# Optimization experiments

Hardware: AMD Instinct MI355X
Metric: run time of the kernel (lower is better)

## Reference

```python
import jax, jax.numpy as jnp
import numpy as np

DT = 10.0 / 200  # 0.05
DX = 20.0 / 128  # 0.15625

# 5x5 fixed finite-difference stencils (torch Conv2d = cross-correlation, so use as-is)
_LAPL = np.array([[0, 0, -1/12, 0, 0],
                  [0, 0,  4/3,  0, 0],
                  [-1/12, 4/3, -5, 4/3, -1/12],
                  [0, 0,  4/3,  0, 0],
                  [0, 0, -1/12, 0, 0]], dtype=np.float32)
_PAR_X = np.array([[0, 0,  1/12, 0, 0],
                   [0, 0, -8/12, 0, 0],
                   [0, 0,  0,    0, 0],
                   [0, 0,  8/12, 0, 0],
                   [0, 0, -1/12, 0, 0]], dtype=np.float32)


def _conv2d_valid(x, kern):
    # x: [N, 1, H, W], kern: [5, 5] -> [N, 1, H-4, W-4]
    return jax.lax.conv_general_dilated(x, jnp.asarray(kern)[None, None], (1, 1), 'VALID')


def _time_deriv(x):
    # x: [T, B, 1, h, w]; central diff interior, one-sided at endpoints (all /DT)
    interior = (x[2:] - x[:-2]) / (2.0 * DT)
    t0 = (-1.5 * x[0] + 2.0 * x[1] - 0.5 * x[2]) / DT
    tn = (0.5 * x[-3] - 2.0 * x[-2] + 1.5 * x[-1]) / DT
    return jnp.concatenate([t0[None], interior, tn[None]], axis=0)


def setup_inputs() -> dict:
    key = jax.random.key(0)
    output = jax.random.normal(key, (20, 8, 3, 256, 256), dtype=jnp.float32)
    return {"output": output}


def reference(output):
    T, B, C, H, W = output.shape
    u = output[:, :, 1:2]  # [T,B,1,H,W]
    v = output[:, :, 2:3]

    lap_u = _conv2d_valid(u.reshape(T * B, 1, H, W), _LAPL).reshape(T, B, 1, H - 4, W - 4) / (DX ** 2)
    lap_v = _conv2d_valid(v.reshape(T * B, 1, H, W), _LAPL).reshape(T, B, 1, H - 4, W - 4) / (DX ** 2)

    uc = u[:, :, :, 2:-2, 2:-2]  # [T,B,1,H-4,W-4]
    vc = v[:, :, :, 2:-2, 2:-2]
    u_t = _time_deriv(uc)
    v_t = _time_deriv(vc)

    Du, Dv = 0.16, 0.08
    f, k = 0.06, 0.062
    f_u = Du * lap_u - uc * vc ** 2 + f * (1.0 - uc) - u_t
    f_v = Dv * lap_v + uc * vc ** 2 - (f + k) * vc - v_t
    return (f_u, f_v)
```

## Files before the change

### kernel.cpp

```cpp
#include <hip/hip_runtime.h>


#define T_OUT (8 * 252 * 252)

typedef float vf4 __attribute__((ext_vector_type(4)));

static __device__ __forceinline__ vf4 lds4u(const float* p) {
    vf4 v;
    __builtin_memcpy(&v, p, 16);
    return v;
}

struct GSRow {
    vf4 u_cm2, u_cm1, u_cc, u_lm1, u_l0;
    vf4 v_cm2, v_cm1, v_cc, v_lm1, v_l0;
};

#define GS_INT(c) { \
    float ut = (ucn.c - s.u_cm1.c) * hdt; \
    float vt = (vcn.c - s.v_cm1.c) * hdt; \
    float uvv = s.u_cc.c * s.v_cc.c * s.v_cc.c; \
    fu.c = Du * s.u_lm1.c - uvv + fR * (1.0f - s.u_cc.c) - ut; \
    fv.c = Dv * s.v_lm1.c + uvv - (fR + kR) * s.v_cc.c - vt; }

#define GS_T0(c) { \
    float ut = (-1.5f * s.u_cm1.c + 2.0f * s.u_cc.c - 0.5f * ucn.c) * inv_dt; \
    float vt = (-1.5f * s.v_cm1.c + 2.0f * s.v_cc.c - 0.5f * vcn.c) * inv_dt; \
    float uvv = s.u_cm1.c * s.v_cm1.c * s.v_cm1.c; \
    fu.c = Du * s.u_l0.c - uvv + fR * (1.0f - s.u_cm1.c) - ut; \
    fv.c = Dv * s.v_l0.c + uvv - (fR + kR) * s.v_cm1.c - vt; }

#define GS_TN(c) { \
    float ut = (0.5f * s.u_cm2.c - 2.0f * s.u_cm1.c + 1.5f * s.u_cc.c) * inv_dt; \
    float vt = (0.5f * s.v_cm2.c - 2.0f * s.v_cm1.c + 1.5f * s.v_cc.c) * inv_dt; \
    float uvv = s.u_cc.c * s.v_cc.c * s.v_cc.c; \
    fu.c = Du * s.u_lm1.c - uvv + fR * (1.0f - s.u_cc.c) - ut; \
    fv.c = Dv * s.v_lm1.c + uvv - (fR + kR) * s.v_cc.c - vt; }

static __device__ __forceinline__ void gs_step(
    const float (*L)[256], int R, int x0, int t, GSRow& s, bool act,
    float* __restrict__ outu, float* __restrict__ outv)
{
    const float C1 = 4.0f / 3.0f, C2 = 1.0f / 12.0f;
    const float inv_dx2 = 1.0f / (0.15625f * 0.15625f);
    const float inv_dt  = 20.0f;
    const float hdt     = 10.0f;
    const float Du = 0.16f, Dv = 0.08f, fR = 0.06f, kR = 0.062f;

    vf4 uL  = *(const vf4*)&L[R + 2][x0];
    vf4 uR  = *(const vf4*)&L[R + 2][x0 + 4];
    vf4 um1 = lds4u(&L[R + 1][x0 + 2]);
    vf4 up1 = lds4u(&L[R + 3][x0 + 2]);
    vf4 um2 = lds4u(&L[R    ][x0 + 2]);
    vf4 up2 = lds4u(&L[R + 4][x0 + 2]);

    vf4 vL  = *(const vf4*)&L[R + 14][x0];
    vf4 vR  = *(const vf4*)&L[R + 14][x0 + 4];
    vf4 vm1 = lds4u(&L[R + 13][x0 + 2]);
    vf4 vp1 = lds4u(&L[R + 15][x0 + 2]);
    vf4 vm2 = lds4u(&L[R + 12][x0 + 2]);
    vf4 vp2 = lds4u(&L[R + 16][x0 + 2]);

    vf4 lu, lv;
    lu.x = (C1*(uL.y + uL.w + um1.x + up1.x) - C2*(uL.x + uR.x + um2.x + up2.x) - 5.0f*uL.z) * inv_dx2;
    lu.y = (C1*(uL.z + uR.x + um1.y + up1.y) - C2*(uL.y + uR.y + um2.y + up2.y) - 5.0f*uL.w) * inv_dx2;
    lu.z = (C1*(uL.w + uR.y + um1.z + up1.z) - C2*(uL.z + uR.z + um2.z + up2.z) - 5.0f*uR.x) * inv_dx2;
    lu.w = (C1*(uR.x + uR.z + um1.w + up1.w) - C2*(uL.w + uR.w + um2.w + up2.w) - 5.0f*uR.y) * inv_dx2;
    lv.x = (C1*(vL.y + vL.w + vm1.x + vp1.x) - C2*(vL.x + vR.x + vm2.x + vp2.x) - 5.0f*vL.z) * inv_dx2;
    lv.y = (C1*(vL.z + vR.x + vm1.y + vp1.y) - C2*(vL.y + vR.y + vm2.y + vp2.y) - 5.0f*vL.w) * inv_dx2;
    lv.z = (C1*(vL.w + vR.y + vm1.z + vp1.z) - C2*(vL.z + vR.z + vm2.z + vp2.z) - 5.0f*vR.x) * inv_dx2;
    lv.w = (C1*(vR.x + vR.z + vm1.w + vp1.w) - C2*(vL.w + vR.w + vm2.w + vp2.w) - 5.0f*vR.y) * inv_dx2;

    vf4 ucn = {uL.z, uL.w, uR.x, uR.y};
    vf4 vcn = {vL.z, vL.w, vR.x, vR.y};

    if (t == 0) { s.u_l0 = lu; s.v_l0 = lv; }

    if (t == 2 && act) {
        vf4 fu, fv;
        GS_T0(x); GS_T0(y); GS_T0(z); GS_T0(w);
        __builtin_nontemporal_store(fu, (vf4*)(outu));
        __builtin_nontemporal_store(fv, (vf4*)(outv));
    }

    if (t >= 2 && act) {
        vf4 fu, fv;
        GS_INT(x); GS_INT(y); GS_INT(z); GS_INT(w);
        __builtin_nontemporal_store(fu, (vf4*)(outu + (size_t)(t - 1) * T_OUT));
        __builtin_nontemporal_store(fv, (vf4*)(outv + (size_t)(t - 1) * T_OUT));
    }

    s.u_cm2 = s.u_cm1; s.u_cm1 = s.u_cc; s.u_cc = ucn; s.u_lm1 = lu;
    s.v_cm2 = s.v_cm1; s.v_cm1 = s.v_cc; s.v_cc = vcn; s.v_lm1 = lv;
}

static __device__ __forceinline__ void gs_tail(
    GSRow& s, bool act, float* __restrict__ outu, float* __restrict__ outv)
{
    const float inv_dt = 20.0f;
    const float Du = 0.16f, Dv = 0.08f, fR = 0.06f, kR = 0.062f;
    if (!act) return;
    vf4 fu, fv;
    GS_TN(x); GS_TN(y); GS_TN(z); GS_TN(w);
    __builtin_nontemporal_store(fu, (vf4*)(outu + (size_t)19 * T_OUT));
    __builtin_nontemporal_store(fv, (vf4*)(outv + (size_t)19 * T_OUT));
}

__global__ __launch_bounds__(256, 1) void gs_loss_kernel(
    const float* __restrict__ in, float* __restrict__ out)
{
    __shared__ float lds[2][24][256];

    const int tid = threadIdx.x;
    const int w   = tid >> 6;
    const int ln  = tid & 63;

    const int b     = blockIdx.x & 7;
    const int ytile = blockIdx.x >> 3;
    const int y0    = ytile * 8;

    const int planeStride = 256 * 256;
    const int bStride     = 3 * planeStride;
    const int tStride     = 24 * planeStride;

    const int col = ln * 4;
    const float* base0 = in + (size_t)b * bStride + planeStride;

    const int gr0 = y0 + w;
    const int gr1 = (y0 + w + 4 < 256) ? (y0 + w + 4) : 255;
    const int gr2 = (y0 + w + 8 < 256) ? (y0 + w + 8) : 255;
    const size_t r0 = (size_t)gr0 * 256 + col;
    const size_t r1 = (size_t)gr1 * 256 + col;
    const size_t r2 = (size_t)gr2 * 256 + col;

    const int x0 = ln * 4;
    const bool active = (ln < 63);
    const bool act2   = active && (y0 + w + 4 < 252);

    const int total = 20 * T_OUT;
    float* outu1 = out + ((size_t)b * 252 + (y0 + w)) * 252 + x0;
    float* outv1 = outu1 + total;
    const int y2 = act2 ? (y0 + w + 4) : (y0 + w);
    float* outu2 = out + ((size_t)b * 252 + y2) * 252 + x0;
    float* outv2 = outu2 + total;

    GSRow s1{}, s2{};

    vf4 sA0, sA1, sA2, sA3, sA4, sA5;
    vf4 sB0, sB1, sB2, sB3, sB4, sB5;

#define ISSUE_A(t) { const float* bt = base0 + (size_t)(t) * tStride; \
    sA0 = *(const vf4*)(bt + r0); \
    sA1 = *(const vf4*)(bt + r1); \
    sA2 = *(const vf4*)(bt + r2); \
    sA3 = *(const vf4*)(bt + planeStride + r0); \
    sA4 = *(const vf4*)(bt + planeStride + r1); \
    sA5 = *(const vf4*)(bt + planeStride + r2); }
#define ISSUE_B(t) { const float* bt = base0 + (size_t)(t) * tStride; \
    sB0 = *(const vf4*)(bt + r0); \
    sB1 = *(const vf4*)(bt + r1); \
    sB2 = *(const vf4*)(bt + r2); \
    sB3 = *(const vf4*)(bt + planeStride + r0); \
    sB4 = *(const vf4*)(bt + planeStride + r1); \
    sB5 = *(const vf4*)(bt + planeStride + r2); }

    ISSUE_A(0);
    ISSUE_B(1);

#pragma unroll
    for (int t = 0; t < 20; ++t) {
        float (*L)[256] = lds[t & 1];

        if ((t & 1) == 0) {
            *(vf4*)&L[w     ][col] = sA0;
            *(vf4*)&L[w + 4 ][col] = sA1;
            *(vf4*)&L[w + 8 ][col] = sA2;
            *(vf4*)&L[w + 12][col] = sA3;
            *(vf4*)&L[w + 16][col] = sA4;
            *(vf4*)&L[w + 20][col] = sA5;
        } else {
            *(vf4*)&L[w     ][col] = sB0;
            *(vf4*)&L[w + 4 ][col] = sB1;
            *(vf4*)&L[w + 8 ][col] = sB2;
            *(vf4*)&L[w + 12][col] = sB3;
            *(vf4*)&L[w + 16][col] = sB4;
            *(vf4*)&L[w + 20][col] = sB5;
        }

        __syncthreads();

        if (t + 2 < 20) {
            if ((t & 1) == 0) { ISSUE_A(t + 2); } else { ISSUE_B(t + 2); }
        }

        gs_step(L, w,     x0, t, s1, active, outu1, outv1);
        gs_step(L, w + 4, x0, t, s2, act2,   outu2, outv2);
    }

    gs_tail(s1, active, outu1, outv1);
    gs_tail(s2, act2,   outu2, outv2);
}

extern "C" void kernel_launch(void* const* d_in, const int* in_sizes, int n_in,
                              void* d_out, int out_size, void* d_ws, size_t ws_size,
                              hipStream_t stream) {
    const float* in = (const float*)d_in[0];
    float* out = (float*)d_out;

    gs_loss_kernel<<<8 * 32, 256, 0, stream>>>(in, out);
}
```

Baseline: 189.5 us.

## Split tiles into column halves, one output row per thread, doubling grid size

```diff
diff --git a/kernel.cpp b/kernel.cpp
--- a/kernel.cpp
+++ b/kernel.cpp
@@ -38,7 +38,7 @@
     fv.c = Dv * s.v_lm1.c + uvv - (fR + kR) * s.v_cc.c - vt; }
 
 static __device__ __forceinline__ void gs_step(
-    const float (*L)[256], int R, int x0, int t, GSRow& s, bool act,
+    const float (*L)[132], int R, int a0, int t, GSRow& s,
     float* __restrict__ outu, float* __restrict__ outv)
 {
     const float C1 = 4.0f / 3.0f, C2 = 1.0f / 12.0f;
@@ -47,19 +47,19 @@
     const float hdt     = 10.0f;
     const float Du = 0.16f, Dv = 0.08f, fR = 0.06f, kR = 0.062f;
 
-    vf4 uL  = *(const vf4*)&L[R + 2][x0];
-    vf4 uR  = *(const vf4*)&L[R + 2][x0 + 4];
-    vf4 um1 = lds4u(&L[R + 1][x0 + 2]);
-    vf4 up1 = lds4u(&L[R + 3][x0 + 2]);
-    vf4 um2 = lds4u(&L[R    ][x0 + 2]);
-    vf4 up2 = lds4u(&L[R + 4][x0 + 2]);
-
-    vf4 vL  = *(const vf4*)&L[R + 14][x0];
-    vf4 vR  = *(const vf4*)&L[R + 14][x0 + 4];
-    vf4 vm1 = lds4u(&L[R + 13][x0 + 2]);
-    vf4 vp1 = lds4u(&L[R + 15][x0 + 2]);
-    vf4 vm2 = lds4u(&L[R + 12][x0 + 2]);
-    vf4 vp2 = lds4u(&L[R + 16][x0 + 2]);
+    vf4 uL  = *(const vf4*)&L[R + 2][a0];
+    vf4 uR  = *(const vf4*)&L[R + 2][a0 + 4];
+    vf4 um1 = lds4u(&L[R + 1][a0 + 2]);
+    vf4 up1 = lds4u(&L[R + 3][a0 + 2]);
+    vf4 um2 = lds4u(&L[R    ][a0 + 2]);
+    vf4 up2 = lds4u(&L[R + 4][a0 + 2]);
+
+    vf4 vL  = *(const vf4*)&L[R + 14][a0];
+    vf4 vR  = *(const vf4*)&L[R + 14][a0 + 4];
+    vf4 vm1 = lds4u(&L[R + 13][a0 + 2]);
+    vf4 vp1 = lds4u(&L[R + 15][a0 + 2]);
+    vf4 vm2 = lds4u(&L[R + 12][a0 + 2]);
+    vf4 vp2 = lds4u(&L[R + 16][a0 + 2]);
 
     vf4 lu, lv;
     lu.x = (C1*(uL.y + uL.w + um1.x + up1.x) - C2*(uL.x + uR.x + um2.x + up2.x) - 5.0f*uL.z) * inv_dx2;
@@ -76,14 +76,14 @@
 
     if (t == 0) { s.u_l0 = lu; s.v_l0 = lv; }
 
-    if (t == 2 && act) {
+    if (t == 2) {
         vf4 fu, fv;
         GS_T0(x); GS_T0(y); GS_T0(z); GS_T0(w);
         __builtin_nontemporal_store(fu, (vf4*)(outu));
         __builtin_nontemporal_store(fv, (vf4*)(outv));
     }
 
-    if (t >= 2 && act) {
+    if (t >= 2) {
         vf4 fu, fv;
         GS_INT(x); GS_INT(y); GS_INT(z); GS_INT(w);
         __builtin_nontemporal_store(fu, (vf4*)(outu + (size_t)(t - 1) * T_OUT));
@@ -94,97 +94,82 @@
     s.v_cm2 = s.v_cm1; s.v_cm1 = s.v_cc; s.v_cc = vcn; s.v_lm1 = lv;
 }
 
-static __device__ __forceinline__ void gs_tail(
-    GSRow& s, bool act, float* __restrict__ outu, float* __restrict__ outv)
-{
-    const float inv_dt = 20.0f;
-    const float Du = 0.16f, Dv = 0.08f, fR = 0.06f, kR = 0.062f;
-    if (!act) return;
-    vf4 fu, fv;
-    GS_TN(x); GS_TN(y); GS_TN(z); GS_TN(w);
-    __builtin_nontemporal_store(fu, (vf4*)(outu + (size_t)19 * T_OUT));
-    __builtin_nontemporal_store(fv, (vf4*)(outv + (size_t)19 * T_OUT));
-}
-
-__global__ __launch_bounds__(256, 1) void gs_loss_kernel(
+__global__ __launch_bounds__(256) void gs_loss_kernel(
     const float* __restrict__ in, float* __restrict__ out)
 {
-    __shared__ float lds[2][24][256];
+    __shared__ float lds[2][24][132];
 
     const int tid = threadIdx.x;
-    const int w   = tid >> 6;
-    const int ln  = tid & 63;
 
     const int b     = blockIdx.x & 7;
-    const int ytile = blockIdx.x >> 3;
+    const int xh    = (blockIdx.x >> 3) & 1;
+    const int ytile = blockIdx.x >> 4;
     const int y0    = ytile * 8;
 
     const int planeStride = 256 * 256;
     const int bStride     = 3 * planeStride;
     const int tStride     = 24 * planeStride;
 
-    const int col = ln * 4;
     const float* base0 = in + (size_t)b * bStride + planeStride;
 
-    const int gr0 = y0 + w;
-    const int gr1 = (y0 + w + 4 < 256) ? (y0 + w + 4) : 255;
-    const int gr2 = (y0 + w + 8 < 256) ? (y0 + w + 8) : 255;
-    const size_t r0 = (size_t)gr0 * 256 + col;
-    const size_t r1 = (size_t)gr1 * 256 + col;
-    const size_t r2 = (size_t)gr2 * 256 + col;
-
-    const int x0 = ln * 4;
-    const bool active = (ln < 63);
-    const bool act2   = active && (y0 + w + 4 < 252);
+    const bool s3 = (tid < 24);
+    int goffs[4], loffs[4];
+#pragma unroll
+    for (int i = 0; i < 4; ++i) {
+        int idx = tid + 256 * i;
+        if (idx >= 792) idx = 791;
+        int r  = idx / 33;
+        int g  = idx - r * 33;
+        int pr = (r < 12) ? r : r - 12;
+        int pl = (r < 12) ? 0 : 1;
+        int gy = y0 + pr; if (gy > 255) gy = 255;
+        goffs[i] = pl * planeStride + gy * 256 + xh * 124 + g * 4;
+        loffs[i] = r * 132 + g * 4;
+    }
+
+    const int R  = tid >> 5;
+    const int cg = tid & 31;
+    const int c0 = xh * 128 + cg * 4;
+    const int a0 = cg * 4 + 4 * xh;
+    const bool act = (c0 <= 248) && (y0 + R < 252);
 
     const int total = 20 * T_OUT;
-    float* outu1 = out + ((size_t)b * 252 + (y0 + w)) * 252 + x0;
-    float* outv1 = outu1 + total;
-    const int y2 = act2 ? (y0 + w + 4) : (y0 + w);
-    float* outu2 = out + ((size_t)b * 252 + y2) * 252 + x0;
-    float* outv2 = outu2 + total;
-
-    GSRow s1{}, s2{};
-
-    vf4 sA0, sA1, sA2, sA3, sA4, sA5;
-    vf4 sB0, sB1, sB2, sB3, sB4, sB5;
+    float* outu = out + ((size_t)b * 252 + (y0 + R)) * 252 + c0;
+    float* outv = outu + total;
+
+    GSRow s{};
+
+    vf4 sA0, sA1, sA2, sA3;
+    vf4 sB0, sB1, sB2, sB3;
 
 #define ISSUE_A(t) { const float* bt = base0 + (size_t)(t) * tStride; \
-    sA0 = *(const vf4*)(bt + r0); \
-    sA1 = *(const vf4*)(bt + r1); \
-    sA2 = *(const vf4*)(bt + r2); \
-    sA3 = *(const vf4*)(bt + planeStride + r0); \
-    sA4 = *(const vf4*)(bt + planeStride + r1); \
-    sA5 = *(const vf4*)(bt + planeStride + r2); }
+    sA0 = *(const vf4*)(bt + goffs[0]); \
+    sA1 = *(const vf4*)(bt + goffs[1]); \
+    sA2 = *(const vf4*)(bt + goffs[2]); \
+    if (s3) sA3 = *(const vf4*)(bt + goffs[3]); }
 #define ISSUE_B(t) { const float* bt = base0 + (size_t)(t) * tStride; \
-    sB0 = *(const vf4*)(bt + r0); \
-    sB1 = *(const vf4*)(bt + r1); \
-    sB2 = *(const vf4*)(bt + r2); \
-    sB3 = *(const vf4*)(bt + planeStride + r0); \
-    sB4 = *(const vf4*)(bt + planeStride + r1); \
-    sB5 = *(const vf4*)(bt + planeStride + r2); }
+    sB0 = *(const vf4*)(bt + goffs[0]); \
+    sB1 = *(const vf4*)(bt + goffs[1]); \
+    sB2 = *(const vf4*)(bt + goffs[2]); \
+    if (s3) sB3 = *(const vf4*)(bt + goffs[3]); }
 
     ISSUE_A(0);
     ISSUE_B(1);
 
 #pragma unroll
     for (int t = 0; t < 20; ++t) {
-        float (*L)[256] = lds[t & 1];
+        float* Lf = &lds[t & 1][0][0];
 
         if ((t & 1) == 0) {
-            *(vf4*)&L[w     ][col] = sA0;
-            *(vf4*)&L[w + 4 ][col] = sA1;
-            *(vf4*)&L[w + 8 ][col] = sA2;
-            *(vf4*)&L[w + 12][col] = sA3;
-            *(vf4*)&L[w + 16][col] = sA4;
-            *(vf4*)&L[w + 20][col] = sA5;
+            *(vf4*)(Lf + loffs[0]) = sA0;
+            *(vf4*)(Lf + loffs[1]) = sA1;
+            *(vf4*)(Lf + loffs[2]) = sA2;
+            if (s3) *(vf4*)(Lf + loffs[3]) = sA3;
         } else {
-            *(vf4*)&L[w     ][col] = sB0;
-            *(vf4*)&L[w + 4 ][col] = sB1;
-            *(vf4*)&L[w + 8 ][col] = sB2;
-            *(vf4*)&L[w + 12][col] = sB3;
-            *(vf4*)&L[w + 16][col] = sB4;
-            *(vf4*)&L[w + 20][col] = sB5;
+            *(vf4*)(Lf + loffs[0]) = sB0;
+            *(vf4*)(Lf + loffs[1]) = sB1;
+            *(vf4*)(Lf + loffs[2]) = sB2;
+            if (s3) *(vf4*)(Lf + loffs[3]) = sB3;
         }
 
         __syncthreads();
@@ -193,12 +178,19 @@
             if ((t & 1) == 0) { ISSUE_A(t + 2); } else { ISSUE_B(t + 2); }
         }
 
-        gs_step(L, w,     x0, t, s1, active, outu1, outv1);
-        gs_step(L, w + 4, x0, t, s2, act2,   outu2, outv2);
-    }
-
-    gs_tail(s1, active, outu1, outv1);
-    gs_tail(s2, act2,   outu2, outv2);
+        if (act) {
+            gs_step(lds[t & 1], R, a0, t, s, outu, outv);
+        }
+    }
+
+    if (act) {
+        const float inv_dt = 20.0f;
+        const float Du = 0.16f, Dv = 0.08f, fR = 0.06f, kR = 0.062f;
+        vf4 fu, fv;
+        GS_TN(x); GS_TN(y); GS_TN(z); GS_TN(w);
+        __builtin_nontemporal_store(fu, (vf4*)(outu + (size_t)19 * T_OUT));
+        __builtin_nontemporal_store(fv, (vf4*)(outv + (size_t)19 * T_OUT));
+    }
 }
 
 extern "C" void kernel_launch(void* const* d_in, const int* in_sizes, int n_in,
@@ -207,5 +199,5 @@
     const float* in = (const float*)d_in[0];
     float* out = (float*)d_out;
 
-    gs_loss_kernel<<<8 * 32, 256, 0, stream>>>(in, out);
-}
+    gs_loss_kernel<<<8 * 2 * 32, 256, 0, stream>>>(in, out);
+}
```

Measured after the change: 194.9 us. 2.8% more time.
